# Kernel tuning notes

Measured on AMD Instinct MI355X. Metric: run time of the kernel, lower is better.

The kernel has to match this reference:

```python
import jax, jax.numpy as jnp
import numpy as np

N, M, E, R, D, H, V, G = 50000, 8, 800000, 8, 128, 128, 32000, 64
NEG_SLOPE = 0.2  # PyG RGATConv default negative_slope


def setup_inputs() -> dict:
    rng = np.random.default_rng(0)
    # ragged entity-index lists per node, padded with -1
    lengths = rng.integers(1, M + 1, size=N)
    idx = rng.integers(0, V, size=(N, M))
    valid = np.arange(M)[None, :] < lengths[:, None]
    x_with_pad = jnp.asarray(np.where(valid, idx, -1).astype(np.int32))
    edge_index = jnp.asarray(rng.integers(0, N, size=(2, E)).astype(np.int32))
    edge_type = jnp.asarray(rng.integers(0, R, size=E).astype(np.int32))
    batch = jnp.asarray(np.sort(rng.integers(0, G, size=N)).astype(np.int32))
    ks = jax.random.split(jax.random.key(0), 12)
    s = 0.05
    return {
        'x_with_pad': x_with_pad,
        'edge_index': edge_index,
        'edge_type': edge_type,
        'batch': batch,
        'embedding_weights': jax.random.normal(ks[0], (V, D), jnp.float32),
        'w1': jax.random.normal(ks[1], (R, D, H), jnp.float32) * s,
        'q1': jax.random.normal(ks[2], (H, 1), jnp.float32) * s,
        'k1': jax.random.normal(ks[3], (H, 1), jnp.float32) * s,
        'b1': jnp.zeros((H,), jnp.float32),
        'w2': jax.random.normal(ks[4], (R, H, H), jnp.float32) * s,
        'q2': jax.random.normal(ks[5], (H, 1), jnp.float32) * s,
        'k2': jax.random.normal(ks[6], (H, 1), jnp.float32) * s,
        'b2': jnp.zeros((H,), jnp.float32),
        'lin_w': jax.random.normal(ks[7], (H, H), jnp.float32) * s,
        'lin_b': jnp.zeros((H,), jnp.float32),
        'num_graphs': G,
    }


def _rgat_conv(x, src, dst, edge_type, w, q, k, b, num_nodes):
    # x: [N, F]; w: [R, F, O]. Per-node per-relation projection, then
    # per-edge gather (same math as PyG's bmm(x[j], w[edge_type]), cheaper).
    xw = jnp.einsum('nf,rfo->nro', x, w)          # [N, R, O]
    out_i = xw[dst, edge_type]                    # [E, O]
    out_j = xw[src, edge_type]                    # [E, O]
    logits = jax.nn.leaky_relu(out_i @ q + out_j @ k, NEG_SLOPE)  # [E, 1]
    # segment softmax over destination nodes (heads=1)
    m = jax.ops.segment_max(logits, dst, num_segments=num_nodes)   # [N, 1]
    e = jnp.exp(logits - m[dst])
    denom = jax.ops.segment_sum(e, dst, num_segments=num_nodes)
    alpha = e / denom[dst]
    msg = alpha * out_j                           # [E, O]
    return jax.ops.segment_sum(msg, dst, num_segments=num_nodes) + b


def reference(x_with_pad, edge_index, edge_type, batch, embedding_weights,
              w1, q1, k1, b1, w2, q2, k2, b2, lin_w, lin_b, num_graphs):
    num_nodes = x_with_pad.shape[0]
    # vectorized ragged gather + mean (replaces the python per-node loop)
    mask = x_with_pad >= 0                                        # [N, M]
    safe = jnp.where(mask, x_with_pad, 0)
    feats = embedding_weights[safe]                               # [N, M, D]
    maskf = mask.astype(feats.dtype)
    x = (feats * maskf[..., None]).sum(1) / maskf.sum(1, keepdims=True)
    src, dst = edge_index[0], edge_index[1]
    x = _rgat_conv(x, src, dst, edge_type, w1, q1, k1, b1, num_nodes)
    x = jax.nn.relu(x)
    x = _rgat_conv(x, src, dst, edge_type, w2, q2, k2, b2, num_nodes)
    x = jax.nn.relu(x)
    x = x @ lin_w.T + lin_b
    return jax.ops.segment_sum(x, batch, num_segments=num_graphs)  # [G, H]
```

## Files before the change

kernel.cpp:

```cpp
#include <hip/hip_runtime.h>
#include <hip/hip_bf16.h>
#include <math.h>

#define D 128

typedef __attribute__((ext_vector_type(4))) float f32x4;
typedef __attribute__((ext_vector_type(8))) short bf16x8;

__device__ inline unsigned short f2bf(float f){
  unsigned u = __float_as_uint(f);
  u += 0x7fffu + ((u >> 16) & 1u);
  return (unsigned short)(u >> 16);
}
__device__ inline float wred_sum(float v){
#pragma unroll
  for (int m = 1; m < 64; m <<= 1) v += __shfl_xor(v, m, 64);
  return v;
}
__device__ inline float wred_max(float v){
#pragma unroll
  for (int m = 1; m < 64; m <<= 1) v = fmaxf(v, __shfl_xor(v, m, 64));
  return v;
}

__global__ __launch_bounds__(256) void k_pool(const int* __restrict__ xpad,
    const float* __restrict__ emb, unsigned short* __restrict__ xo, int N, int M){
  int wv = threadIdx.x >> 6, ln = threadIdx.x & 63;
  int n = blockIdx.x * 4 + wv;
  if (n >= N) return;
  const int4* xr = (const int4*)(xpad + n * M);
  int4 ia = xr[0], ib = xr[1];
  int cnt = (ia.x >= 0) + (ia.y >= 0) + (ia.z >= 0) + (ia.w >= 0)
          + (ib.x >= 0) + (ib.y >= 0) + (ib.z >= 0) + (ib.w >= 0);
  float2 acc = {0.f, 0.f};
#define POOL_ONE(idx) if ((idx) >= 0){ \
    float2 v = ((const float2*)(emb + (size_t)(idx) * D))[ln]; \
    acc.x += v.x; acc.y += v.y; }
  POOL_ONE(ia.x) POOL_ONE(ia.y) POOL_ONE(ia.z) POOL_ONE(ia.w)
  POOL_ONE(ib.x) POOL_ONE(ib.y) POOL_ONE(ib.z) POOL_ONE(ib.w)
#undef POOL_ONE
  float inv = 1.f / (float)cnt;
  unsigned u = ((unsigned)f2bf(acc.y * inv) << 16) | f2bf(acc.x * inv);
  *(unsigned*)(xo + (size_t)n * D + 2 * ln) = u;
}

__global__ void k_count(const int* __restrict__ dst, int* __restrict__ cnt, int E){
  int e = blockIdx.x * 256 + threadIdx.x;
  if (e < E) atomicAdd(&cnt[dst[e]], 1);
}

__global__ __launch_bounds__(256) void k_scan_blk(const int* __restrict__ cc,
    int* __restrict__ bsum, int nb){
  __shared__ int sh[256];
  int base = blockIdx.x * 1024 + threadIdx.x * 4;
  int s = 0;
#pragma unroll
  for (int j = 0; j < 4; ++j){
    int i = base + j;
    if (i < nb) s += cc[i];
  }
  sh[threadIdx.x] = s; __syncthreads();
  for (int off = 128; off > 0; off >>= 1){
    if (threadIdx.x < off) sh[threadIdx.x] += sh[threadIdx.x + off];
    __syncthreads();
  }
  if (threadIdx.x == 0) bsum[blockIdx.x] = sh[0];
}

__global__ __launch_bounds__(1024) void k_scan_top(const int* __restrict__ bsum,
    int* __restrict__ boff, int* __restrict__ rp, int nblk, int nb){
  __shared__ int sh[1024];
  int t = threadIdx.x;
  int v = (t < nblk) ? bsum[t] : 0;
  sh[t] = v; __syncthreads();
  for (int off = 1; off < 1024; off <<= 1){
    int a = sh[t];
    int b = (t >= off) ? sh[t - off] : 0;
    __syncthreads();
    sh[t] = a + b;
    __syncthreads();
  }
  if (t < nblk) boff[t] = sh[t] - v;
  if (t == 1023) rp[nb] = sh[1023];
}

__global__ __launch_bounds__(256) void k_scan_fin(int* __restrict__ cc,
    const int* __restrict__ boff, int* __restrict__ rp, int nb){
  __shared__ int sh[256];
  int t = threadIdx.x;
  int base = blockIdx.x * 1024 + t * 4;
  int c[4]; int local = 0;
#pragma unroll
  for (int j = 0; j < 4; ++j){
    int i = base + j;
    c[j] = (i < nb) ? cc[i] : 0;
    local += c[j];
  }
  sh[t] = local; __syncthreads();
  for (int off = 1; off < 256; off <<= 1){
    int a = sh[t];
    int b = (t >= off) ? sh[t - off] : 0;
    __syncthreads();
    sh[t] = a + b;
    __syncthreads();
  }
  int run = sh[t] - local + boff[blockIdx.x];
#pragma unroll
  for (int j = 0; j < 4; ++j){
    int i = base + j;
    if (i < nb){ rp[i] = run; cc[i] = run; run += c[j]; }
  }
}

__global__ void k_scatter(const int* __restrict__ src, const int* __restrict__ dst,
    const int* __restrict__ et, int* __restrict__ cur, int* __restrict__ pack, int E){
  int e = blockIdx.x * 256 + threadIdx.x;
  if (e < E){
    int p = atomicAdd(&cur[dst[e]], 1);
    pack[p] = (et[e] << 27) | src[e];
  }
}

__global__ void k_wtr(const float* __restrict__ w, unsigned short* __restrict__ wbf, int total){
  int id = blockIdx.x * 256 + threadIdx.x;
  if (id >= total) return;
  int d = id & 127, h = (id >> 7) & 127, r = id >> 14;
  wbf[id] = f2bf(w[(size_t)r * 16384 + d * 128 + h]);
}

__global__ void k_cvt(const float* __restrict__ s, unsigned short* __restrict__ dd, int total){
  int id = blockIdx.x * 256 + threadIdx.x;
  if (id < total) dd[id] = f2bf(s[id]);
}

__global__ __launch_bounds__(256) void k_xw(const unsigned short* __restrict__ x,
    const unsigned short* __restrict__ wbf,
    const float* __restrict__ qv, const float* __restrict__ kv,
    unsigned short* __restrict__ xw,
    float* __restrict__ aT, float* __restrict__ bT,
    int N, int R, int nwg){
  __shared__ __align__(16) char smem[32768];
  unsigned short (*wt)[128] = (unsigned short (*)[128])smem;
  unsigned short (*ot)[136] = (unsigned short (*)[136])smem;
  int wv = threadIdx.x >> 6, ln = threadIdx.x & 63;
  int g = ln >> 4, m16 = ln & 15;
  int orig = blockIdx.x;
  int q = nwg >> 3, rm = nwg & 7;
  int xcd = orig & 7, idx = orig >> 3;
  int wgid = (xcd < rm ? xcd * (q + 1) : rm * (q + 1) + (xcd - rm) * q) + idx;
  int r    = wgid % 8;
  int tile = wgid / 8;
  int n0 = tile * 64;
  int nA = n0 + wv * 16 + m16;
  {
    const uint4* wsrc = (const uint4*)(wbf + (size_t)r * 16384);
    for (int i = threadIdx.x; i < 2048; i += 256){
      int h = i >> 4, c = i & 15;
      *(uint4*)&wt[h][(c ^ (h & 15)) * 8] = wsrc[i];
    }
  }
  bf16x8 af[4];
#pragma unroll
  for (int kc = 0; kc < 4; ++kc) af[kc] = (bf16x8){0,0,0,0,0,0,0,0};
  if (nA < N){
#pragma unroll
    for (int kc = 0; kc < 4; ++kc)
      af[kc] = *(const bf16x8*)(x + (size_t)nA * D + kc * 32 + g * 8);
  }
  __syncthreads();
  f32x4 acc[8];
#pragma unroll
  for (int i = 0; i < 8; ++i) acc[i] = (f32x4){0.f, 0.f, 0.f, 0.f};
#pragma unroll
  for (int kc = 0; kc < 4; ++kc){
#pragma unroll
    for (int hf = 0; hf < 8; ++hf){
      bf16x8 bfr = *(const bf16x8*)&wt[hf * 16 + m16][((kc * 4 + g) ^ m16) * 8];
      acc[hf] = __builtin_amdgcn_mfma_f32_16x16x32_bf16(af[kc], bfr, acc[hf], 0, 0, 0);
    }
  }
  {
    float qr[8], kr[8];
#pragma unroll
    for (int hf = 0; hf < 8; ++hf){ qr[hf] = qv[hf * 16 + m16]; kr[hf] = kv[hf * 16 + m16]; }
#pragma unroll
    for (int jj = 0; jj < 4; ++jj){
      float pa = 0.f, pb = 0.f;
#pragma unroll
      for (int hf = 0; hf < 8; ++hf){
        pa += acc[hf][jj] * qr[hf];
        pb += acc[hf][jj] * kr[hf];
      }
#pragma unroll
      for (int mm = 1; mm < 16; mm <<= 1){
        pa += __shfl_xor(pa, mm, 64);
        pb += __shfl_xor(pb, mm, 64);
      }
      if (m16 == 0){
        int n = n0 + wv * 16 + g * 4 + jj;
        if (n < N){ aT[n * R + r] = pa; bT[n * R + r] = pb; }
      }
    }
  }
  __syncthreads();
#pragma unroll
  for (int hf = 0; hf < 8; ++hf){
#pragma unroll
    for (int jj = 0; jj < 4; ++jj){
      ot[wv * 16 + g * 4 + jj][hf * 16 + m16] = f2bf(acc[hf][jj]);
    }
  }
  __syncthreads();
  unsigned short* dstp = xw + ((size_t)r * N + n0) * 128;
  int limit = (N - n0 < 64) ? (N - n0) * 16 : 1024;
  for (int i = threadIdx.x; i < limit; i += 256){
    int row = i >> 4, c16 = i & 15;
    *(uint4*)(dstp + row * 128 + c16 * 8) = *(const uint4*)&ot[row][c16 * 8];
  }
}

__global__ __launch_bounds__(256) void k_alpha(const int* __restrict__ rp,
    const int* __restrict__ pack, const float* __restrict__ aT, const float* __restrict__ bT,
    float* __restrict__ alp, float* __restrict__ denom, int N, int R){
  int wv = threadIdx.x >> 6, ln = threadIdx.x & 63;
  int n = blockIdx.x * 4 + wv;
  if (n >= N) return;
  int beg = rp[n], end = rp[n + 1];
  if (end <= beg) return;
  float mx = -3.4e38f;
  for (int i = beg + ln; i < end; i += 64){
    int v = pack[i]; int t = v >> 27; int s = v & 0x7ffffff;
    float l = aT[n * R + t] + bT[s * R + t];
    l = l > 0.f ? l : 0.2f * l;
    alp[i] = l;
    mx = fmaxf(mx, l);
  }
  mx = wred_max(mx);
  float sm = 0.f;
  for (int i = beg + ln; i < end; i += 64){
    float ev = __expf(alp[i] - mx);
    alp[i] = ev; sm += ev;
  }
  sm = wred_sum(sm);
  if (ln == 0) denom[n] = 1.f / sm;
}

__global__ __launch_bounds__(256) void k_aggX(const unsigned short* __restrict__ xw,
    const int* __restrict__ rp, const int* __restrict__ pack, const float* __restrict__ alp,
    const float* __restrict__ denom, const float* __restrict__ bias,
    unsigned short* __restrict__ xo, int N, int R){
  int wv = threadIdx.x >> 6, ln = threadIdx.x & 63;
  int n = blockIdx.x * 4 + wv;
  if (n >= N) return;
  int beg = rp[n], end = rp[n + 1];
  float2 s0 = {0.f, 0.f}, s1 = {0.f, 0.f}, s2 = {0.f, 0.f}, s3 = {0.f, 0.f};
  int i = beg;
  for (; i + 3 < end; i += 4){
    int v0 = pack[i], v1 = pack[i + 1], v2 = pack[i + 2], v3 = pack[i + 3];
    float al0 = alp[i], al1 = alp[i + 1], al2 = alp[i + 2], al3 = alp[i + 3];
    unsigned u0 = *(const unsigned*)(xw + ((size_t)(v0 >> 27) * N + (v0 & 0x7ffffff)) * 128 + 2 * ln);
    unsigned u1 = *(const unsigned*)(xw + ((size_t)(v1 >> 27) * N + (v1 & 0x7ffffff)) * 128 + 2 * ln);
    unsigned u2 = *(const unsigned*)(xw + ((size_t)(v2 >> 27) * N + (v2 & 0x7ffffff)) * 128 + 2 * ln);
    unsigned u3 = *(const unsigned*)(xw + ((size_t)(v3 >> 27) * N + (v3 & 0x7ffffff)) * 128 + 2 * ln);
    s0.x += al0 * __uint_as_float(u0 << 16);
    s0.y += al0 * __uint_as_float(u0 & 0xffff0000u);
    s1.x += al1 * __uint_as_float(u1 << 16);
    s1.y += al1 * __uint_as_float(u1 & 0xffff0000u);
    s2.x += al2 * __uint_as_float(u2 << 16);
    s2.y += al2 * __uint_as_float(u2 & 0xffff0000u);
    s3.x += al3 * __uint_as_float(u3 << 16);
    s3.y += al3 * __uint_as_float(u3 & 0xffff0000u);
  }
  for (; i < end; ++i){
    int v0 = pack[i];
    float al0 = alp[i];
    unsigned u0 = *(const unsigned*)(xw + ((size_t)(v0 >> 27) * N + (v0 & 0x7ffffff)) * 128 + 2 * ln);
    s0.x += al0 * __uint_as_float(u0 << 16);
    s0.y += al0 * __uint_as_float(u0 & 0xffff0000u);
  }
  float dn = (end > beg) ? denom[n] : 0.f;
  float ox = fmaxf((s0.x + s1.x + s2.x + s3.x) * dn + bias[2 * ln], 0.f);
  float oy = fmaxf((s0.y + s1.y + s2.y + s3.y) * dn + bias[2 * ln + 1], 0.f);
  unsigned u = ((unsigned)f2bf(oy) << 16) | f2bf(ox);
  *(unsigned*)(xo + (size_t)n * D + 2 * ln) = u;
}

__global__ __launch_bounds__(256) void k_final(const unsigned short* __restrict__ x,
    const unsigned short* __restrict__ lwbf, const float* __restrict__ lb,
    const int* __restrict__ batch, float* __restrict__ out, int N){
  __shared__ unsigned short wt[128][136];
  __shared__ float st[64][129];
  __shared__ int bsh[64];
  {
    const uint4* src = (const uint4*)lwbf;
    for (int i = threadIdx.x; i < 2048; i += 256){
      int h = i >> 4, kblk = i & 15;
      *(uint4*)&wt[h][kblk * 8] = src[i];
    }
  }
  __syncthreads();
  int wv = threadIdx.x >> 6, ln = threadIdx.x & 63;
  int g = ln >> 4, m16 = ln & 15;
  int n0 = blockIdx.x * 64;
  int nA = n0 + wv * 16 + m16;
  f32x4 acc[8];
#pragma unroll
  for (int i = 0; i < 8; ++i) acc[i] = (f32x4){0.f, 0.f, 0.f, 0.f};
#pragma unroll
  for (int kc = 0; kc < 4; ++kc){
    bf16x8 af = (bf16x8){0,0,0,0,0,0,0,0};
    if (nA < N) af = *(const bf16x8*)(x + (size_t)nA * D + kc * 32 + g * 8);
#pragma unroll
    for (int hf = 0; hf < 8; ++hf){
      bf16x8 bfr = *(const bf16x8*)&wt[hf * 16 + m16][kc * 32 + g * 8];
      acc[hf] = __builtin_amdgcn_mfma_f32_16x16x32_bf16(af, bfr, acc[hf], 0, 0, 0);
    }
  }
#pragma unroll
  for (int hf = 0; hf < 8; ++hf){
    int h = hf * 16 + m16;
    float bv = lb[h];
#pragma unroll
    for (int jj = 0; jj < 4; ++jj){
      int row = wv * 16 + g * 4 + jj;
      int n = n0 + row;
      st[row][h] = (n < N) ? (acc[hf][jj] + bv) : 0.f;
    }
  }
  if (threadIdx.x < 64){
    int n = n0 + threadIdx.x;
    bsh[threadIdx.x] = (n < N) ? batch[n] : -1;
  }
  __syncthreads();
  if (threadIdx.x < 128){
    int h = threadIdx.x;
    int lastValid = (N - n0 < 64) ? (N - n0 - 1) : 63;
    int cg = bsh[0];
    float sum = 0.f;
    for (int row = 0; row <= lastValid; ++row){
      int bg = bsh[row];
      if (bg != cg){
        atomicAdd(&out[(size_t)cg * D + h], sum);
        sum = 0.f; cg = bg;
      }
      sum += st[row][h];
    }
    atomicAdd(&out[(size_t)cg * D + h], sum);
  }
}

extern "C" void kernel_launch(void* const* d_in, const int* in_sizes, int n_in,
                              void* d_out, int out_size, void* d_ws, size_t ws_size,
                              hipStream_t stream){
  const int*   xpad  = (const int*)d_in[0];
  const int*   eidx  = (const int*)d_in[1];
  const int*   etyp  = (const int*)d_in[2];
  const int*   batch = (const int*)d_in[3];
  const float* emb   = (const float*)d_in[4];
  const float* w1    = (const float*)d_in[5];
  const float* q1    = (const float*)d_in[6];
  const float* k1    = (const float*)d_in[7];
  const float* b1    = (const float*)d_in[8];
  const float* w2    = (const float*)d_in[9];
  const float* q2    = (const float*)d_in[10];
  const float* k2    = (const float*)d_in[11];
  const float* b2    = (const float*)d_in[12];
  const float* lw    = (const float*)d_in[13];
  const float* lb    = (const float*)d_in[14];

  int N = in_sizes[3];
  int M = in_sizes[0] / N;
  int E = in_sizes[2];
  int R = in_sizes[5] / (128 * 128);
  const int* esrc = eidx;
  const int* edst = eidx + E;

  char* p = (char*)d_ws;
  auto carve = [&](size_t b) -> void* {
    void* q = (void*)p; p += (b + 255) & ~(size_t)255; return q;
  };
  unsigned short* x_a = (unsigned short*)carve((size_t)N * D * 2);
  unsigned short* x_b = (unsigned short*)carve((size_t)N * D * 2);
  float* aT   = (float*)carve((size_t)N * R * 4);
  float* bT   = (float*)carve((size_t)N * R * 4);
  float* dnm  = (float*)carve((size_t)N * 4);
  int*   rp   = (int*)carve((size_t)(N + 1) * 4);
  int*   cur  = (int*)carve((size_t)N * 4);
  int*   pack = (int*)carve((size_t)E * 4);
  float* alp  = (float*)carve((size_t)E * 4);
  unsigned short* wbf1 = (unsigned short*)carve((size_t)R * 128 * 128 * 2);
  unsigned short* wbf2 = (unsigned short*)carve((size_t)R * 128 * 128 * 2);
  unsigned short* lwbf = (unsigned short*)carve((size_t)128 * 128 * 2);
  int* bsum = (int*)carve((size_t)4096 * 4);
  int* boff = (int*)carve((size_t)4096 * 4);
  if ((size_t)(p - (char*)d_ws) > ws_size) return;
  unsigned short* xw = (unsigned short*)carve((size_t)N * R * 128 * 2);
  if ((size_t)(p - (char*)d_ws) > ws_size) return;

  hipMemsetAsync(cur, 0, (size_t)N * 4, stream);
  hipMemsetAsync(d_out, 0, (size_t)out_size * 4, stream);

  int eg = (E + 255) / 256;
  int nblk = (N + 1023) / 1024;
  k_count   <<<eg, 256, 0, stream>>>(edst, cur, E);
  k_scan_blk<<<nblk, 256, 0, stream>>>(cur, bsum, N);
  k_scan_top<<<1, 1024, 0, stream>>>(bsum, boff, rp, nblk, N);
  k_scan_fin<<<nblk, 256, 0, stream>>>(cur, boff, rp, N);
  k_scatter <<<eg, 256, 0, stream>>>(esrc, edst, etyp, cur, pack, E);

  int wtot = R * 128 * 128;
  k_wtr<<<(wtot + 255) / 256, 256, 0, stream>>>(w1, wbf1, wtot);
  k_wtr<<<(wtot + 255) / 256, 256, 0, stream>>>(w2, wbf2, wtot);
  k_cvt<<<(128 * 128 + 255) / 256, 256, 0, stream>>>(lw, lwbf, 128 * 128);

  int ng4 = (N + 3) / 4;
  int ntile = (N + 63) / 64;
  int nwg = ntile * R;
  k_pool<<<ng4, 256, 0, stream>>>(xpad, emb, x_a, N, M);

  k_xw   <<<nwg, 256, 0, stream>>>(x_a, wbf1, q1, k1, xw, aT, bT, N, R, nwg);
  k_alpha<<<ng4, 256, 0, stream>>>(rp, pack, aT, bT, alp, dnm, N, R);
  k_aggX <<<ng4, 256, 0, stream>>>(xw, rp, pack, alp, dnm, b1, x_b, N, R);

  k_xw   <<<nwg, 256, 0, stream>>>(x_b, wbf2, q2, k2, xw, aT, bT, N, R, nwg);
  k_alpha<<<ng4, 256, 0, stream>>>(rp, pack, aT, bT, alp, dnm, N, R);
  k_aggX <<<ng4, 256, 0, stream>>>(xw, rp, pack, alp, dnm, b2, x_a, N, R);

  k_final<<<ntile, 256, 0, stream>>>(x_a, lwbf, lb, batch, (float*)d_out, N);
}
```

Before: 351.8 us.

## Replace atomic CSR scatter with two-pass coarse binning via shared-memory staging

```diff
diff --git a/kernel.cpp b/kernel.cpp
--- a/kernel.cpp
+++ b/kernel.cpp
@@ -112,12 +112,75 @@
   }
 }
 
-__global__ void k_scatter(const int* __restrict__ src, const int* __restrict__ dst,
-    const int* __restrict__ et, int* __restrict__ cur, int* __restrict__ pack, int E){
-  int e = blockIdx.x * 256 + threadIdx.x;
-  if (e < E){
-    int p = atomicAdd(&cur[dst[e]], 1);
-    pack[p] = (et[e] << 27) | src[e];
+__global__ void k_initcur(const int* __restrict__ rp, int* __restrict__ coarse_cur, int NBk){
+  int b = threadIdx.x;
+  if (b < NBk) coarse_cur[b] = rp[b * 256];
+}
+
+__global__ __launch_bounds__(256) void k_binA(const int* __restrict__ src,
+    const int* __restrict__ dst, const int* __restrict__ et,
+    int* __restrict__ coarse_cur, int2* __restrict__ tmp, int E){
+  __shared__ int lcnt[256], lscan[256], loff[256], gbase[256];
+  __shared__ int2 stage[2048];
+  __shared__ int staddr[2048];
+  int t = threadIdx.x;
+  int e0 = blockIdx.x * 2048;
+  lcnt[t] = 0; loff[t] = 0;
+  __syncthreads();
+  int word[8], dd[8], cb[8]; bool val[8];
+#pragma unroll
+  for (int j = 0; j < 8; ++j){
+    int e = e0 + t + j * 256;
+    val[j] = (e < E);
+    if (val[j]){
+      dd[j] = dst[e];
+      word[j] = (et[e] << 27) | src[e];
+      cb[j] = dd[j] >> 8;
+      atomicAdd(&lcnt[cb[j]], 1);
+    }
+  }
+  __syncthreads();
+  int v = lcnt[t];
+  lscan[t] = v; __syncthreads();
+  for (int off = 1; off < 256; off <<= 1){
+    int a = lscan[t];
+    int b = (t >= off) ? lscan[t - off] : 0;
+    __syncthreads();
+    lscan[t] = a + b;
+    __syncthreads();
+  }
+  int excl = lscan[t] - v;
+  if (v > 0) gbase[t] = atomicAdd(&coarse_cur[t], v);
+  lscan[t] = excl;
+  __syncthreads();
+#pragma unroll
+  for (int j = 0; j < 8; ++j){
+    if (val[j]){
+      int k = atomicAdd(&loff[cb[j]], 1);
+      int s = lscan[cb[j]] + k;
+      stage[s]  = make_int2(word[j], dd[j]);
+      staddr[s] = gbase[cb[j]] + k;
+    }
+  }
+  __syncthreads();
+  int tot = lscan[255] + lcnt[255];
+  for (int s = t; s < tot; s += 256){
+    tmp[staddr[s]] = stage[s];
+  }
+}
+
+__global__ __launch_bounds__(256) void k_binB(const int* __restrict__ rp,
+    const int2* __restrict__ tmp, int* __restrict__ pack, int N){
+  __shared__ int lcur[256];
+  int nbase = blockIdx.x * 256;
+  int nend = nbase + 256; if (nend > N) nend = N;
+  int ebeg = rp[nbase], eend = rp[nend];
+  lcur[threadIdx.x] = 0;
+  __syncthreads();
+  for (int i = ebeg + threadIdx.x; i < eend; i += 256){
+    int2 v = tmp[i];
+    int k = atomicAdd(&lcur[v.y - nbase], 1);
+    pack[rp[v.y] + k] = v.x;
   }
 }
 
@@ -388,6 +451,8 @@
   int*   cur  = (int*)carve((size_t)N * 4);
   int*   pack = (int*)carve((size_t)E * 4);
   float* alp  = (float*)carve((size_t)E * 4);
+  int2*  tmp  = (int2*)carve((size_t)E * 8);
+  int*   ccur = (int*)carve((size_t)256 * 4);
   unsigned short* wbf1 = (unsigned short*)carve((size_t)R * 128 * 128 * 2);
   unsigned short* wbf2 = (unsigned short*)carve((size_t)R * 128 * 128 * 2);
   unsigned short* lwbf = (unsigned short*)carve((size_t)128 * 128 * 2);
@@ -402,11 +467,15 @@
 
   int eg = (E + 255) / 256;
   int nblk = (N + 1023) / 1024;
+  int NBk = (N + 255) / 256;
+  int nbinA = (E + 2047) / 2048;
   k_count   <<<eg, 256, 0, stream>>>(edst, cur, E);
   k_scan_blk<<<nblk, 256, 0, stream>>>(cur, bsum, N);
   k_scan_top<<<1, 1024, 0, stream>>>(bsum, boff, rp, nblk, N);
   k_scan_fin<<<nblk, 256, 0, stream>>>(cur, boff, rp, N);
-  k_scatter <<<eg, 256, 0, stream>>>(esrc, edst, etyp, cur, pack, E);
+  k_initcur <<<1, 256, 0, stream>>>(rp, ccur, NBk);
+  k_binA    <<<nbinA, 256, 0, stream>>>(esrc, edst, etyp, ccur, tmp, E);
+  k_binB    <<<NBk, 256, 0, stream>>>(rp, tmp, pack, N);
 
   int wtot = R * 128 * 128;
   k_wtr<<<(wtot + 255) / 256, 256, 0, stream>>>(w1, wbf1, wtot);
```

After: 322.6 us. -8.3%, faster.
